# Kernel optimization log

Measured on AMD Instinct MI355X. Metric: run time of the kernel, lower is better.

Reference implementation:

```python
import jax, jax.numpy as jnp
import numpy as np

N = 20000      # nodes
E = 640000     # edges
FIN = 256
FQK = 256


def setup_inputs() -> dict:
    key = jax.random.key(0)
    kx, ks, kd, kw = jax.random.split(key, 4)
    x = jax.random.normal(kx, (N, FIN), dtype=jnp.float32)
    # src must be sorted (original scatter_softmax assumes grouped index);
    # force last element to N-1 so nbatches == N as in batch[-1]+1.
    src = jnp.sort(jax.random.randint(ks, (E,), 0, N))
    src = src.at[-1].set(N - 1)
    dest = jax.random.randint(kd, (E,), 0, N)
    ei = jnp.stack([src, dest]).astype(jnp.int64)
    # nn.Linear(Fin, 2*Fqk, bias=False) weight: [2*Fqk, Fin]
    bound = 1.0 / np.sqrt(FIN)
    W = jax.random.uniform(kw, (2 * FQK, FIN), dtype=jnp.float32,
                           minval=-bound, maxval=bound)
    return {"x": x, "ei": ei, "W": W}


def reference(x, ei, W):
    src, dest = ei[0], ei[1]
    n_nodes = x.shape[0]
    scaling = FQK ** -0.5
    qk = x @ W.T                      # [N, 2*Fqk]
    q, k = jnp.split(qk, 2, axis=-1)  # each [N, Fqk]
    q = q * scaling
    # per-edge dot product: (q[src] . k[dest])  -> [E]
    aw = jnp.einsum('ef,ef->e', q[src], k[dest])
    # scatter softmax over edges grouped by src node (raw exp, as original)
    ex = jnp.exp(aw)
    expsum = jax.ops.segment_sum(ex, src, num_segments=n_nodes)  # [N]
    return ex / expsum[src]
```

## Files before the change

### kernel.cpp

```cpp
#include <hip/hip_runtime.h>
#include <cmath>

#define FIN 256
#define FQK 256
#define SCALING 0.0625f
#define MAX_SEG 256
#define ASTRIDE 264

typedef __bf16 bf16_t;
typedef bf16_t bf16x8 __attribute__((ext_vector_type(8)));
typedef float  f32x4  __attribute__((ext_vector_type(4)));

__device__ __forceinline__ unsigned short f2bf(float f) {
    unsigned int u = __float_as_uint(f);
    u += 0x7FFFu + ((u >> 16) & 1u);
    return (unsigned short)(u >> 16);
}
__device__ __forceinline__ float bf_lo(unsigned int w) { return __uint_as_float(w << 16); }
__device__ __forceinline__ float bf_hi(unsigned int w) { return __uint_as_float(w & 0xFFFF0000u); }

__device__ __forceinline__ bf16x8 cvt8(float4 a, float4 b) {
    bf16x8 r;
    r[0] = (bf16_t)a.x; r[1] = (bf16_t)a.y; r[2] = (bf16_t)a.z; r[3] = (bf16_t)a.w;
    r[4] = (bf16_t)b.x; r[5] = (bf16_t)b.y; r[6] = (bf16_t)b.z; r[7] = (bf16_t)b.w;
    return r;
}

__global__ __launch_bounds__(256) void m_seg_kernel(const float* __restrict__ W,
                                                    unsigned short* __restrict__ MbF,
                                                    const int* __restrict__ src,
                                                    int* __restrict__ seg, int N, int E) {
    const int b = blockIdx.x;
    if (b < FIN) {
        const int f = b;
        const int k = threadIdx.x;
        const float* __restrict__ Wq = W;
        const float* __restrict__ Wk = W + FQK * FIN;
        float acc = 0.f;
#pragma unroll 8
        for (int c = 0; c < FQK; ++c)
            acc += Wq[c * FIN + f] * Wk[c * FIN + k];
        const int ft  = f >> 4, m16 = f & 15;
        const int kcI = k >> 5, q = (k >> 3) & 3, e = k & 7;
        MbF[(size_t)(((kcI * 16 + ft) * 64 + q * 16 + m16) * 8 + e)] = f2bf(acc * SCALING);
    } else {
        const int n = (b - FIN) * 256 + threadIdx.x;
        if (n > N) return;
        int lo = 0, hi = E;
        while (lo < hi) {
            const int mid = (lo + hi) >> 1;
            if (src[mid] < n) lo = mid + 1; else hi = mid;
        }
        seg[n] = lo;
    }
}

__global__ __launch_bounds__(256) void gemm_y_kernel(const float* __restrict__ x,
                                                     const unsigned short* __restrict__ MbF,
                                                     unsigned short* __restrict__ y, int N) {
    __shared__ unsigned short sA[32 * ASTRIDE];

    const int t    = threadIdx.x;
    const int wv   = t >> 6;
    const int lane = t & 63;
    const int q    = lane >> 4;
    const int m16  = lane & 15;
    const int n0   = blockIdx.x * 32;
    const int f0   = wv * 64;

    {
        const int srow = t >> 3;
        const int scol = (t & 7) * 32;
        const int n    = n0 + srow;
        const int nc   = n < N ? n : N - 1;
        const float* __restrict__ xp = x + (size_t)nc * FIN + scol;
        unsigned short* __restrict__ sp = &sA[srow * ASTRIDE + scol];
#pragma unroll
        for (int u = 0; u < 4; ++u) {
            const float4 a = *(const float4*)(xp + u * 8);
            const float4 b = *(const float4*)(xp + u * 8 + 4);
            *(bf16x8*)(sp + u * 8) = cvt8(a, b);
        }
    }
    __syncthreads();

    f32x4 acc[2][4] = {};

#pragma unroll
    for (int kc = 0; kc < FIN; kc += 32) {
        bf16x8 afrag[2];
#pragma unroll
        for (int mt = 0; mt < 2; ++mt)
            afrag[mt] = *(const bf16x8*)&sA[(mt * 16 + m16) * ASTRIDE + kc + q * 8];

        const unsigned short* __restrict__ bp =
            MbF + (size_t)(((kc >> 5) * 16 + (f0 >> 4)) * 64 + lane) * 8;
#pragma unroll
        for (int ft = 0; ft < 4; ++ft) {
            union { uint4 u; bf16x8 v; } bu;
            bu.u = *(const uint4*)(bp + ft * 512);
#pragma unroll
            for (int mt = 0; mt < 2; ++mt)
                acc[mt][ft] = __builtin_amdgcn_mfma_f32_16x16x32_bf16(afrag[mt], bu.v,
                                                                     acc[mt][ft], 0, 0, 0);
        }
    }

#pragma unroll
    for (int mt = 0; mt < 2; ++mt) {
#pragma unroll
        for (int r = 0; r < 4; ++r) {
            const int n = n0 + mt * 16 + q * 4 + r;
            if (n < N) {
#pragma unroll
                for (int ft = 0; ft < 4; ++ft)
                    y[(size_t)n * FIN + f0 + ft * 16 + m16] = f2bf(acc[mt][ft][r]);
            }
        }
    }
}

__device__ __forceinline__ float dot8(uint4 qv, float4 xa, float4 xb) {
    return bf_lo(qv.x) * xa.x + bf_hi(qv.x) * xa.y
         + bf_lo(qv.y) * xa.z + bf_hi(qv.y) * xa.w
         + bf_lo(qv.z) * xb.x + bf_hi(qv.z) * xb.y
         + bf_lo(qv.w) * xb.z + bf_hi(qv.w) * xb.w;
}

__global__ __launch_bounds__(256) void node_edge_kernel(const float* __restrict__ x,
                                                        const unsigned short* __restrict__ y,
                                                        const int* __restrict__ dest,
                                                        const int* __restrict__ seg,
                                                        float* __restrict__ out, int N) {
    __shared__ float exlds[4][MAX_SEG];

    const int w    = threadIdx.x >> 6;
    const int lane = threadIdx.x & 63;
    const int n    = blockIdx.x * 4 + w;
    const int g    = lane >> 3;
    const int j    = lane & 7;

    int   s0 = 0, cnt = 0;
    float inv = 0.f;

    if (n < N) {
        s0  = seg[n];
        cnt = seg[n + 1] - s0;
    }

    if (cnt > 0) {
        float4 xf[8];
        const float* __restrict__ xr = x + (size_t)n * FIN + j * 32;
#pragma unroll
        for (int u = 0; u < 8; ++u) xf[u] = *(const float4*)(xr + u * 4);

        float sum = 0.f;
        const int nit = (cnt + 7) >> 3;

        uint4 c0, c1, c2, c3;
        bool vc = g < cnt;
        if (vc) {
            const int d = dest[s0 + g];
            const uint4* __restrict__ yr = (const uint4*)(y + (size_t)d * FIN) + j * 4;
            c0 = yr[0]; c1 = yr[1]; c2 = yr[2]; c3 = yr[3];
        }

        for (int it = 0; it < nit; ++it) {
            const int i   = it * 8 + g;
            const int inx = i + 8;
            const bool vn = inx < cnt;
            uint4 p0, p1, p2, p3;
            if (vn) {
                const int d = dest[s0 + inx];
                const uint4* __restrict__ yr = (const uint4*)(y + (size_t)d * FIN) + j * 4;
                p0 = yr[0]; p1 = yr[1]; p2 = yr[2]; p3 = yr[3];
            }
            if (vc) {
                float acc = dot8(c0, xf[0], xf[1]) + dot8(c1, xf[2], xf[3])
                          + dot8(c2, xf[4], xf[5]) + dot8(c3, xf[6], xf[7]);
                acc += __shfl_xor(acc, 1, 64);
                acc += __shfl_xor(acc, 2, 64);
                acc += __shfl_xor(acc, 4, 64);
                const float ex = __expf(acc);
                sum += ex;
                if (j == 0 && i < MAX_SEG) exlds[w][i] = ex;
            }
            c0 = p0; c1 = p1; c2 = p2; c3 = p3; vc = vn;
        }
        sum += __shfl_xor(sum, 8, 64);
        sum += __shfl_xor(sum, 16, 64);
        sum += __shfl_xor(sum, 32, 64);
        inv = 1.0f / sum;
    }

    __syncthreads();

    if (cnt > 0) {
        const int lim = cnt < MAX_SEG ? cnt : MAX_SEG;
        for (int i = lane; i < lim; i += 64)
            out[s0 + i] = exlds[w][i] * inv;
    }
}

extern "C" void kernel_launch(void* const* d_in, const int* in_sizes, int n_in,
                              void* d_out, int out_size, void* d_ws, size_t ws_size,
                              hipStream_t stream) {
    const float* x  = (const float*)d_in[0];
    const int*   ei = (const int*)d_in[1];
    const float* W  = (const float*)d_in[2];
    float* out = (float*)d_out;

    const int N = in_sizes[0] / FIN;
    const int E = in_sizes[1] / 2;

    unsigned short* MbF = (unsigned short*)d_ws;
    unsigned short* y   = MbF + (size_t)FIN * FIN;
    int*            seg = (int*)(y + (size_t)N * FIN);

    const int segBlocks = (N + 256) / 256;
    m_seg_kernel<<<FIN + segBlocks, 256, 0, stream>>>(W, MbF, ei, seg, N, E);

    gemm_y_kernel<<<(N + 31) / 32, 256, 0, stream>>>(x, MbF, y, N);

    node_edge_kernel<<<(N + 3) / 4, 256, 0, stream>>>(x, y, ei + E, seg, out, N);
}
```

Before: 137.1 us.

## Deepen gather prefetch to three stages and coalesce GEMM loads/stores via LDS

The edge kernel's gather loop moves from one-ahead to three-deep prefetching with rotating register buffers, so more dependent y-row loads are in flight per wave. The dot product uses packed two-wide FMAs, and the block-wide barrier is dropped in favour of early exits per wave. The GEMM now loads x with fully coalesced row-major accesses and stages the bf16 output tile through LDS so y is written with 16-byte stores instead of scattered 2-byte stores. The deeper prefetch raises register pressure and may lower occupancy. Removing the barrier relies on each wave only reading its own LDS slice, which is safe within a wave.

```diff
diff --git a/kernel.cpp b/kernel.cpp
--- a/kernel.cpp
+++ b/kernel.cpp
@@ -10,6 +10,7 @@
 typedef __bf16 bf16_t;
 typedef bf16_t bf16x8 __attribute__((ext_vector_type(8)));
 typedef float  f32x4  __attribute__((ext_vector_type(4)));
+typedef float  f32x2  __attribute__((ext_vector_type(2)));
 
 __device__ __forceinline__ unsigned short f2bf(float f) {
     unsigned int u = __float_as_uint(f);
@@ -69,17 +70,17 @@
     const int f0   = wv * 64;
 
     {
-        const int srow = t >> 3;
-        const int scol = (t & 7) * 32;
-        const int n    = n0 + srow;
-        const int nc   = n < N ? n : N - 1;
-        const float* __restrict__ xp = x + (size_t)nc * FIN + scol;
-        unsigned short* __restrict__ sp = &sA[srow * ASTRIDE + scol];
-#pragma unroll
-        for (int u = 0; u < 4; ++u) {
-            const float4 a = *(const float4*)(xp + u * 8);
-            const float4 b = *(const float4*)(xp + u * 8 + 4);
-            *(bf16x8*)(sp + u * 8) = cvt8(a, b);
+        const int rsub = t >> 5;
+        const int col  = (t & 31) * 8;
+#pragma unroll
+        for (int p = 0; p < 4; ++p) {
+            const int r  = p * 8 + rsub;
+            const int n  = n0 + r;
+            const int nc = n < N ? n : N - 1;
+            const float* __restrict__ xp = x + (size_t)nc * FIN + col;
+            const float4 a = *(const float4*)(xp);
+            const float4 b = *(const float4*)(xp + 4);
+            *(bf16x8*)&sA[r * ASTRIDE + col] = cvt8(a, b);
         }
     }
     __syncthreads();
@@ -106,25 +107,40 @@
         }
     }
 
-#pragma unroll
-    for (int mt = 0; mt < 2; ++mt) {
-#pragma unroll
-        for (int r = 0; r < 4; ++r) {
-            const int n = n0 + mt * 16 + q * 4 + r;
-            if (n < N) {
-#pragma unroll
-                for (int ft = 0; ft < 4; ++ft)
-                    y[(size_t)n * FIN + f0 + ft * 16 + m16] = f2bf(acc[mt][ft][r]);
-            }
-        }
-    }
-}
-
-__device__ __forceinline__ float dot8(uint4 qv, float4 xa, float4 xb) {
-    return bf_lo(qv.x) * xa.x + bf_hi(qv.x) * xa.y
-         + bf_lo(qv.y) * xa.z + bf_hi(qv.y) * xa.w
-         + bf_lo(qv.z) * xb.x + bf_hi(qv.z) * xb.y
-         + bf_lo(qv.w) * xb.z + bf_hi(qv.w) * xb.w;
+    __syncthreads();
+#pragma unroll
+    for (int mt = 0; mt < 2; ++mt)
+#pragma unroll
+        for (int r = 0; r < 4; ++r)
+#pragma unroll
+            for (int ft = 0; ft < 4; ++ft)
+                sA[(mt * 16 + q * 4 + r) * ASTRIDE + f0 + ft * 16 + m16] =
+                    f2bf(acc[mt][ft][r]);
+    __syncthreads();
+
+#pragma unroll
+    for (int s = 0; s < 4; ++s) {
+        const int row = s * 8 + (t >> 5);
+        const int c16 = t & 31;
+        const int n   = n0 + row;
+        if (n < N) {
+            const uint4 v = *(const uint4*)&sA[row * ASTRIDE + c16 * 8];
+            *(uint4*)(y + (size_t)n * FIN + c16 * 8) = v;
+        }
+    }
+}
+
+__device__ __forceinline__ f32x2 dotp(unsigned int wq, float xl, float xh, f32x2 acc) {
+    f32x2 e;  e[0] = bf_lo(wq); e[1] = bf_hi(wq);
+    f32x2 xx; xx[0] = xl;       xx[1] = xh;
+    return __builtin_elementwise_fma(e, xx, acc);
+}
+__device__ __forceinline__ f32x2 dot8v(uint4 qv, float4 xa, float4 xb, f32x2 acc) {
+    acc = dotp(qv.x, xa.x, xa.y, acc);
+    acc = dotp(qv.y, xa.z, xa.w, acc);
+    acc = dotp(qv.z, xb.x, xb.y, acc);
+    acc = dotp(qv.w, xb.z, xb.w, acc);
+    return acc;
 }
 
 __global__ __launch_bounds__(256) void node_edge_kernel(const float* __restrict__ x,
@@ -140,66 +156,91 @@
     const int g    = lane >> 3;
     const int j    = lane & 7;
 
-    int   s0 = 0, cnt = 0;
-    float inv = 0.f;
-
-    if (n < N) {
-        s0  = seg[n];
-        cnt = seg[n + 1] - s0;
-    }
-
-    if (cnt > 0) {
-        float4 xf[8];
+    if (n >= N) return;
+    const int s0  = seg[n];
+    const int cnt = seg[n + 1] - s0;
+    if (cnt <= 0) return;
+
+    float4 xf[8];
+    {
         const float* __restrict__ xr = x + (size_t)n * FIN + j * 32;
 #pragma unroll
         for (int u = 0; u < 8; ++u) xf[u] = *(const float4*)(xr + u * 4);
-
-        float sum = 0.f;
-        const int nit = (cnt + 7) >> 3;
-
-        uint4 c0, c1, c2, c3;
-        bool vc = g < cnt;
-        if (vc) {
-            const int d = dest[s0 + g];
-            const uint4* __restrict__ yr = (const uint4*)(y + (size_t)d * FIN) + j * 4;
-            c0 = yr[0]; c1 = yr[1]; c2 = yr[2]; c3 = yr[3];
-        }
-
-        for (int it = 0; it < nit; ++it) {
-            const int i   = it * 8 + g;
-            const int inx = i + 8;
-            const bool vn = inx < cnt;
-            uint4 p0, p1, p2, p3;
-            if (vn) {
-                const int d = dest[s0 + inx];
-                const uint4* __restrict__ yr = (const uint4*)(y + (size_t)d * FIN) + j * 4;
-                p0 = yr[0]; p1 = yr[1]; p2 = yr[2]; p3 = yr[3];
-            }
-            if (vc) {
-                float acc = dot8(c0, xf[0], xf[1]) + dot8(c1, xf[2], xf[3])
-                          + dot8(c2, xf[4], xf[5]) + dot8(c3, xf[6], xf[7]);
-                acc += __shfl_xor(acc, 1, 64);
-                acc += __shfl_xor(acc, 2, 64);
-                acc += __shfl_xor(acc, 4, 64);
-                const float ex = __expf(acc);
-                sum += ex;
-                if (j == 0 && i < MAX_SEG) exlds[w][i] = ex;
-            }
-            c0 = p0; c1 = p1; c2 = p2; c3 = p3; vc = vn;
-        }
-        sum += __shfl_xor(sum, 8, 64);
-        sum += __shfl_xor(sum, 16, 64);
-        sum += __shfl_xor(sum, 32, 64);
-        inv = 1.0f / sum;
-    }
-
-    __syncthreads();
-
-    if (cnt > 0) {
-        const int lim = cnt < MAX_SEG ? cnt : MAX_SEG;
-        for (int i = lane; i < lim; i += 64)
-            out[s0 + i] = exlds[w][i] * inv;
-    }
+    }
+
+    float sum = 0.f;
+
+#define DCLAMP(d) ((unsigned)(d) < (unsigned)N ? (d) : 0)
+
+#define GISSUE(B0, B1, B2, B3, d, valid)                                       \
+    if (valid) {                                                               \
+        const uint4* __restrict__ yr =                                         \
+            (const uint4*)(y + (size_t)DCLAMP(d) * FIN) + j * 4;               \
+        B0 = yr[0]; B1 = yr[1]; B2 = yr[2]; B3 = yr[3];                        \
+    }
+
+#define CONSUME(B0, B1, B2, B3, idx, valid)                                    \
+    if (valid) {                                                               \
+        f32x2 a2 = {0.f, 0.f};                                                 \
+        a2 = dot8v(B0, xf[0], xf[1], a2);                                      \
+        a2 = dot8v(B1, xf[2], xf[3], a2);                                      \
+        a2 = dot8v(B2, xf[4], xf[5], a2);                                      \
+        a2 = dot8v(B3, xf[6], xf[7], a2);                                      \
+        float accv = a2[0] + a2[1];                                            \
+        accv += __shfl_xor(accv, 1, 64);                                       \
+        accv += __shfl_xor(accv, 2, 64);                                       \
+        accv += __shfl_xor(accv, 4, 64);                                       \
+        const float ex = __expf(accv);                                         \
+        sum += ex;                                                             \
+        if (j == 0 && (idx) < MAX_SEG) exlds[w][idx] = ex;                     \
+    }
+
+    uint4 A0 = {}, A1 = {}, A2 = {}, A3 = {};
+    uint4 B0 = {}, B1 = {}, B2 = {}, B3 = {};
+    uint4 C0 = {}, C1 = {}, C2 = {}, C3 = {};
+
+    int  iA = g, iB = g + 8, iC = g + 16;
+    bool vA = iA < cnt, vB = iB < cnt, vC = iC < cnt;
+
+    {
+        const int dA = vA ? dest[s0 + iA] : 0;
+        GISSUE(A0, A1, A2, A3, dA, vA);
+        const int dB = vB ? dest[s0 + iB] : 0;
+        GISSUE(B0, B1, B2, B3, dB, vB);
+        const int dC = vC ? dest[s0 + iC] : 0;
+        GISSUE(C0, C1, C2, C3, dC, vC);
+    }
+    int inext = g + 24;
+    int dN    = (inext < cnt) ? dest[s0 + inext] : 0;
+
+    const int nit = (cnt + 7) >> 3;
+    for (int it = 0; it < nit; it += 3) {
+        CONSUME(A0, A1, A2, A3, iA, vA);
+        iA = inext; vA = iA < cnt;
+        GISSUE(A0, A1, A2, A3, dN, vA);
+        inext += 8; dN = (inext < cnt) ? dest[s0 + inext] : 0;
+        CONSUME(B0, B1, B2, B3, iB, vB);
+        iB = inext; vB = iB < cnt;
+        GISSUE(B0, B1, B2, B3, dN, vB);
+        inext += 8; dN = (inext < cnt) ? dest[s0 + inext] : 0;
+        CONSUME(C0, C1, C2, C3, iC, vC);
+        iC = inext; vC = iC < cnt;
+        GISSUE(C0, C1, C2, C3, dN, vC);
+        inext += 8; dN = (inext < cnt) ? dest[s0 + inext] : 0;
+    }
+
+    sum += __shfl_xor(sum, 8, 64);
+    sum += __shfl_xor(sum, 16, 64);
+    sum += __shfl_xor(sum, 32, 64);
+    const float inv = 1.0f / sum;
+
+    const int lim = cnt < MAX_SEG ? cnt : MAX_SEG;
+    for (int i = lane; i < lim; i += 64)
+        out[s0 + i] = exlds[w][i] * inv;
+
+#undef GISSUE
+#undef CONSUME
+#undef DCLAMP
 }
 
 extern "C" void kernel_launch(void* const* d_in, const int* in_sizes, int n_in,
```

Result: slower. 140.8 us (+2.7%).
